# Performance work log

Hardware: AMD Instinct MI355X
Metric: run time of the kernel (lower is better)

## Reference

```python
import jax, jax.numpy as jnp
from jax import lax
import numpy as np

B, N, NPOINT, NSAMPLE, C = 4, 8192, 2048, 32, 128
RADIUS = 0.2
H1, H2, OUT = 64, 128, 128  # mlp: (3+C)->H1->H2, sas: H2->OUT


def fps(xyz, npoint):
    # furthest point sampling: xyz (B,N,3) -> idx (B,npoint) int32
    b, n, _ = xyz.shape
    init_idx = jnp.zeros((b,), jnp.int32)

    def step(carry, _):
        dist, last = carry
        p = jnp.take_along_axis(xyz, last[:, None, None], axis=1)  # (B,1,3)
        d = jnp.sum((xyz - p) ** 2, axis=-1)                       # (B,N)
        dist = jnp.minimum(dist, d)
        nxt = jnp.argmax(dist, axis=-1).astype(jnp.int32)
        return (dist, nxt), nxt

    (_, _), rest = lax.scan(step, (jnp.full((b, n), 1e10, jnp.float32), init_idx),
                            None, length=npoint - 1)
    return jnp.concatenate([init_idx[None, :], rest], axis=0).T    # (B,npoint)


def ball_query(xyz, new_xyz, radius, nsample):
    # xyz (B,N,3), new_xyz (B,S,3) -> idx (B,S,nsample) int32
    n = xyz.shape[1]
    d2 = jnp.sum((new_xyz[:, :, None, :] - xyz[:, None, :, :]) ** 2, axis=-1)  # (B,S,N)
    ar = jnp.arange(n, dtype=jnp.int32)
    keys = jnp.where(d2 <= radius * radius, ar, n)  # valid -> own index, invalid -> N
    neg_vals, _ = lax.top_k(-keys, nsample)          # smallest nsample keys
    idx = -neg_vals
    first = idx[..., :1]
    return jnp.where(idx >= n, first, idx)           # pad invalid with first valid


def gather_points(pts, idx):
    # pts (B,N,D), idx (B,S,ns) -> (B,S,ns,D)
    b, s, ns = idx.shape
    flat = jnp.take_along_axis(pts, idx.reshape(b, s * ns, 1), axis=1)
    return flat.reshape(b, s, ns, -1)


def setup_inputs() -> dict:
    key = jax.random.key(0)
    ks = jax.random.split(key, 8)
    xyz = jax.random.uniform(ks[0], (B, N, 3), dtype=jnp.float32)
    features = jax.random.normal(ks[1], (B, C, N), dtype=jnp.float32)
    cin = C + 3
    W1 = jax.random.normal(ks[2], (H1, cin), dtype=jnp.float32) / np.sqrt(cin)
    b1 = jnp.zeros((H1,), jnp.float32)
    W2 = jax.random.normal(ks[3], (H2, H1), dtype=jnp.float32) / np.sqrt(H1)
    b2 = jnp.zeros((H2,), jnp.float32)
    Wsa = jax.random.normal(ks[4], (OUT, H2), dtype=jnp.float32) / np.sqrt(H2)
    bsa = jnp.zeros((OUT,), jnp.float32)
    return {"xyz": xyz, "features": features, "W1": W1, "b1": b1,
            "W2": W2, "b2": b2, "Wsa": Wsa, "bsa": bsa}


def reference(xyz, features, W1, b1, W2, b2, Wsa, bsa):
    center_idx = fps(xyz, NPOINT)                                   # (B,S)
    new_xyz = jnp.take_along_axis(xyz, center_idx[:, :, None], axis=1)  # (B,S,3)
    g_idx = ball_query(xyz, new_xyz, RADIUS, NSAMPLE)               # (B,S,ns)
    g_xyz = gather_points(xyz, g_idx) - new_xyz[:, :, None, :]      # (B,S,ns,3) relative coords
    g_feat = gather_points(features.transpose(0, 2, 1), g_idx)      # (B,S,ns,C)
    h = jnp.concatenate([g_xyz, g_feat], axis=-1)                   # (B,S,ns,3+C)
    h = jax.nn.relu(jnp.einsum('bsnc,oc->bsno', h, W1) + b1)        # shared 1x1-conv MLP
    h = jax.nn.relu(jnp.einsum('bsnc,oc->bsno', h, W2) + b2)
    pooled = jnp.max(h, axis=2)                                     # max over nsample -> (B,S,H2)
    out = jnp.einsum('bsc,oc->bso', pooled, Wsa) + bsa              # sas channel mixer
    return new_xyz, out.transpose(0, 2, 1)                          # (B,S,3), (B,OUT,S)
```

## Files before the change

### kernel.cpp

```cpp
#include <hip/hip_runtime.h>
#include <cstdint>
#include <cstddef>

#define NB 4
#define NN 8192
#define NPTS 2048
#define NSAMP 32
#define NC 128
#define CIN 131
#define NH1 64
#define NH2 128
#define NOUTC 128
#define GCELLS 4096

typedef float v2f __attribute__((ext_vector_type(2)));

__device__ __forceinline__ float d2_exact(float ax, float ay, float az,
                                          float bx, float by, float bz) {
  float dx = ax - bx, dy = ay - by, dz = az - bz;
  return __fadd_rn(__fadd_rn(__fmul_rn(dx, dx), __fmul_rn(dy, dy)),
                   __fmul_rn(dz, dz));
}

#if __has_builtin(__builtin_amdgcn_mov_dpp)
template <int CTRL>
__device__ __forceinline__ float dppf(float v) {
  return __int_as_float(
      __builtin_amdgcn_mov_dpp(__float_as_int(v), CTRL, 0xF, 0xF, true));
}
template <int CTRL>
__device__ __forceinline__ int dppi(int v) {
  return __builtin_amdgcn_mov_dpp(v, CTRL, 0xF, 0xF, true);
}
#else
template <int CTRL>
__device__ __forceinline__ float dppf(float v) {
  const int m = (CTRL == 0xB1) ? 1 : (CTRL == 0x4E) ? 2 : (CTRL == 0x141) ? 7 : 15;
  return __shfl_xor(v, m);
}
template <int CTRL>
__device__ __forceinline__ int dppi(int v) {
  const int m = (CTRL == 0xB1) ? 1 : (CTRL == 0x4E) ? 2 : (CTRL == 0x141) ? 7 : 15;
  return __shfl_xor(v, m);
}
#endif

__device__ __forceinline__ bool tgt(float av, int ai, float bv, int bi) {
  return (av > bv) || (av == bv && ai < bi);
}

__device__ __forceinline__ void red_pair(float& bv, int& bi, float ov, int oi) {
  bool t = tgt(ov, oi, bv, bi);
  bv = t ? ov : bv;
  bi = t ? oi : bi;
}
template <int CTRL>
__device__ __forceinline__ void red5(float& v, int& i, float& x, float& y,
                                     float& z) {
  float ov = dppf<CTRL>(v);
  int oi = dppi<CTRL>(i);
  float ox = dppf<CTRL>(x), oy = dppf<CTRL>(y), oz = dppf<CTRL>(z);
  bool t = tgt(ov, oi, v, i);
  v = t ? ov : v; i = t ? oi : i;
  x = t ? ox : x; y = t ? oy : y; z = t ? oz : z;
}

__device__ __forceinline__ int spread3(int v) {
  return (v & 1) | ((v & 2) << 2) | ((v & 4) << 4) | ((v & 8) << 6);
}

__global__ __launch_bounds__(1024, 1) void sort_kernel(
    const float* __restrict__ xyz, float* __restrict__ xs,
    float* __restrict__ ys, float* __restrict__ zs, int* __restrict__ io) {
  __shared__ int hist[GCELLS];
  __shared__ int cbase[GCELLS];
  __shared__ int wtot[16];
  __shared__ int woff[16];
  const int b = blockIdx.x;
  const int tid = threadIdx.x;
  const int lane = tid & 63;
  const int wid = tid >> 6;
  const float* xb = xyz + (size_t)b * NN * 3;
  for (int i = tid; i < GCELLS; i += 1024) hist[i] = 0;
  __syncthreads();
  int cell[8];
  float px[8], py[8], pz[8];
#pragma unroll
  for (int k = 0; k < 8; ++k) {
    int j = tid + (k << 10);
    float x = xb[j * 3 + 0], y = xb[j * 3 + 1], z = xb[j * 3 + 2];
    px[k] = x; py[k] = y; pz[k] = z;
    int cx = min(15, max(0, (int)(x * 16.0f)));
    int cy = min(15, max(0, (int)(y * 16.0f)));
    int cz = min(15, max(0, (int)(z * 16.0f)));
    cell[k] = spread3(cx) | (spread3(cy) << 1) | (spread3(cz) << 2);
    atomicAdd(&hist[cell[k]], 1);
  }
  __syncthreads();
  const int i0 = tid * 4;
  int h0 = hist[i0], h1 = hist[i0 + 1], h2 = hist[i0 + 2], h3 = hist[i0 + 3];
  int s4 = h0 + h1 + h2 + h3;
  int v = s4;
#pragma unroll
  for (int d = 1; d < 64; d <<= 1) {
    int o = __shfl_up(v, d);
    if (lane >= d) v += o;
  }
  if (lane == 63) wtot[wid] = v;
  __syncthreads();
  if (tid < 16) {
    int acc = 0;
    for (int w = 0; w < 16; ++w) {
      if (w == tid) woff[tid] = acc;
      acc += wtot[w];
    }
  }
  __syncthreads();
  int eb = woff[wid] + v - s4;
  cbase[i0] = eb;
  cbase[i0 + 1] = eb + h0;
  cbase[i0 + 2] = eb + h0 + h1;
  cbase[i0 + 3] = eb + h0 + h1 + h2;
  __syncthreads();
  for (int i = tid; i < GCELLS; i += 1024) hist[i] = 0;
  __syncthreads();
  const size_t bo = (size_t)b * NN;
#pragma unroll
  for (int k = 0; k < 8; ++k) {
    int pos = cbase[cell[k]] + atomicAdd(&hist[cell[k]], 1);
    xs[bo + pos] = px[k];
    ys[bo + pos] = py[k];
    zs[bo + pos] = pz[k];
    io[bo + pos] = tid + (k << 10);
  }
}

__global__ __launch_bounds__(1024, 1) void fps_kernel(
    const float* __restrict__ xyz, const float* __restrict__ xs,
    const float* __restrict__ ys, const float* __restrict__ zs,
    const int* __restrict__ io, float* __restrict__ newxyz) {
#pragma clang fp contract(off)
  const int b = blockIdx.x;
  const int tid = threadIdx.x;
  const int lane = tid & 63;
  const int wid = tid >> 6;
  const size_t bo = (size_t)b * NN;

  float X[8], Y[8], Z[8], D[8];
  int I[8];
  float gcx, gcy, gcz, gr;
  {
    float mx = 0.f, my = 0.f, mz = 0.f;
#pragma unroll
    for (int k = 0; k < 8; ++k) {
      int s = tid * 8 + k;
      X[k] = xs[bo + s];
      Y[k] = ys[bo + s];
      Z[k] = zs[bo + s];
      I[k] = io[bo + s];
      D[k] = 1e30f;
      mx += X[k]; my += Y[k]; mz += Z[k];
    }
    mx *= 0.125f; my *= 0.125f; mz *= 0.125f;
    float r2m = 0.f;
#pragma unroll
    for (int k = 0; k < 8; ++k)
      r2m = fmaxf(r2m, d2_exact(X[k], Y[k], Z[k], mx, my, mz));
    gcx = mx; gcy = my; gcz = mz;
    gr = __fmul_rn(sqrtf(r2m), 1.0001f) + 1e-6f;
  }
  float gv = -1.0f;
  int gidx = 0x7fffffff;
  float gx = 0.f, gy = 0.f, gz = 0.f;
  float T = 3e38f;
  float cv = -1.0f; int ci = 0x7fffffff;
  float ccx = 0.f, ccy = 0.f, ccz = 0.f;

  __shared__ float sv[2][16];
  __shared__ int si[2][16];
  __shared__ float sxx[2][16], syy[2][16], szz[2][16];

  const float* xb = xyz + (size_t)b * NN * 3;
  float cx = xb[0], cy = xb[1], cz = xb[2];
  if (tid == 0) {
    newxyz[(size_t)b * NPTS * 3 + 0] = cx;
    newxyz[(size_t)b * NPTS * 3 + 1] = cy;
    newxyz[(size_t)b * NPTS * 3 + 2] = cz;
  }

  for (int t = 1; t < NPTS; ++t) {
    const int par = t & 1;
    const float d2c = d2_exact(gcx, gcy, gcz, cx, cy, cz);
    const bool dirty = d2c < T;
    if (__ballot(dirty) != 0ull) {
      float nv = -1.f; int ni = 0x7fffffff;
      float nx = 0.f, ny = 0.f, nz = 0.f;
#pragma unroll
      for (int k = 0; k < 8; ++k) {
        float dd = d2_exact(X[k], Y[k], Z[k], cx, cy, cz);
        float nd = fminf(D[k], dd);
        D[k] = nd;
        bool c = tgt(nd, I[k], nv, ni);
        nv = c ? nd : nv; ni = c ? I[k] : ni;
        nx = c ? X[k] : nx; ny = c ? Y[k] : ny; nz = c ? Z[k] : nz;
      }
      gv = nv; gidx = ni; gx = nx; gy = ny; gz = nz;
      float s = __fadd_rn(__fmul_rn(sqrtf(gv), 1.0001f),
                          __fadd_rn(gr, 2e-3f));
      T = __fmul_rn(__fmul_rn(s, s), 1.0001f);
      float rv = gv; int ri = gidx;
      red_pair(rv, ri, dppf<0xB1>(rv), dppi<0xB1>(ri));
      red_pair(rv, ri, dppf<0x4E>(rv), dppi<0x4E>(ri));
      red_pair(rv, ri, dppf<0x141>(rv), dppi<0x141>(ri));
      red_pair(rv, ri, dppf<0x140>(rv), dppi<0x140>(ri));
      red_pair(rv, ri, __shfl_xor(rv, 16), __shfl_xor(ri, 16));
      red_pair(rv, ri, __shfl_xor(rv, 32), __shfl_xor(ri, 32));
      unsigned long long m = __ballot(gidx == ri);
      int owner = (int)__builtin_ctzll(m);
      cv = rv; ci = ri;
      ccx = __shfl(gx, owner);
      ccy = __shfl(gy, owner);
      ccz = __shfl(gz, owner);
    }
    if (lane == 0) {
      sv[par][wid] = cv; si[par][wid] = ci;
      sxx[par][wid] = ccx; syy[par][wid] = ccy; szz[par][wid] = ccz;
    }
    __syncthreads();
    const int sl = lane & 15;
    float v = sv[par][sl];
    int i = si[par][sl];
    float xx = sxx[par][sl], yy = syy[par][sl], zz = szz[par][sl];
    red5<0xB1>(v, i, xx, yy, zz);
    red5<0x4E>(v, i, xx, yy, zz);
    red5<0x141>(v, i, xx, yy, zz);
    red5<0x140>(v, i, xx, yy, zz);
    cx = xx; cy = yy; cz = zz;
    if (gidx == i) {
      size_t o = ((size_t)b * NPTS + t) * 3;
      newxyz[o + 0] = xx; newxyz[o + 1] = yy; newxyz[o + 2] = zz;
    }
  }
}

__global__ __launch_bounds__(1024, 1) void fps_nosort_kernel(
    const float* __restrict__ xyz, float* __restrict__ newxyz) {
#pragma clang fp contract(off)
  const int b = blockIdx.x;
  const int tid = threadIdx.x;
  const int lane = tid & 63;
  const int wid = tid >> 6;
  const float* xb = xyz + (size_t)b * NN * 3;
  v2f x2[4], y2[4], z2[4], dd[4];
#pragma unroll
  for (int p = 0; p < 4; ++p) {
    int j0 = tid + ((2 * p) << 10);
    int j1 = tid + ((2 * p + 1) << 10);
    x2[p].x = xb[j0 * 3 + 0]; x2[p].y = xb[j1 * 3 + 0];
    y2[p].x = xb[j0 * 3 + 1]; y2[p].y = xb[j1 * 3 + 1];
    z2[p].x = xb[j0 * 3 + 2]; z2[p].y = xb[j1 * 3 + 2];
    dd[p].x = 1e10f; dd[p].y = 1e10f;
  }
  __shared__ float vbuf[2][16];
  __shared__ int ibuf[2][16];
  __shared__ float cbuf[2][16][3];
  float cx = xb[0], cy = xb[1], cz = xb[2];
  if (tid == 0) {
    newxyz[(size_t)b * NPTS * 3 + 0] = cx;
    newxyz[(size_t)b * NPTS * 3 + 1] = cy;
    newxyz[(size_t)b * NPTS * 3 + 2] = cz;
  }
  for (int t = 1; t < NPTS; ++t) {
    const int par = t & 1;
    float bv = -1.0f; int bi = 0;
    float bwx = 0.f, bwy = 0.f, bwz = 0.f;
#pragma unroll
    for (int p = 0; p < 4; ++p) {
      v2f dx = x2[p] - (v2f){cx, cx};
      v2f dy = y2[p] - (v2f){cy, cy};
      v2f dz = z2[p] - (v2f){cz, cz};
      v2f s = dx * dx + dy * dy + dz * dz;
      v2f nd;
      nd.x = fminf(dd[p].x, s.x);
      nd.y = fminf(dd[p].y, s.y);
      dd[p] = nd;
      { bool c = nd.x > bv;
        bv = c ? nd.x : bv; bi = c ? (tid + ((2 * p) << 10)) : bi;
        bwx = c ? x2[p].x : bwx; bwy = c ? y2[p].x : bwy; bwz = c ? z2[p].x : bwz; }
      { bool c = nd.y > bv;
        bv = c ? nd.y : bv; bi = c ? (tid + ((2 * p + 1) << 10)) : bi;
        bwx = c ? x2[p].y : bwx; bwy = c ? y2[p].y : bwy; bwz = c ? z2[p].y : bwz; }
    }
    red_pair(bv, bi, dppf<0xB1>(bv), dppi<0xB1>(bi));
    red_pair(bv, bi, dppf<0x4E>(bv), dppi<0x4E>(bi));
    red_pair(bv, bi, dppf<0x141>(bv), dppi<0x141>(bi));
    red_pair(bv, bi, dppf<0x140>(bv), dppi<0x140>(bi));
    red_pair(bv, bi, __shfl_xor(bv, 16), __shfl_xor(bi, 16));
    red_pair(bv, bi, __shfl_xor(bv, 32), __shfl_xor(bi, 32));
    if (tid == (bi & 1023)) {
      vbuf[par][wid] = bv; ibuf[par][wid] = bi;
      cbuf[par][wid][0] = bwx; cbuf[par][wid][1] = bwy; cbuf[par][wid][2] = bwz;
    }
    __syncthreads();
    float v2w = vbuf[par][lane & 15];
    int i2w = ibuf[par][lane & 15];
    red_pair(v2w, i2w, dppf<0xB1>(v2w), dppi<0xB1>(i2w));
    red_pair(v2w, i2w, dppf<0x4E>(v2w), dppi<0x4E>(i2w));
    red_pair(v2w, i2w, dppf<0x141>(v2w), dppi<0x141>(i2w));
    red_pair(v2w, i2w, dppf<0x140>(v2w), dppi<0x140>(i2w));
    const int slot = (i2w & 1023) >> 6;
    cx = cbuf[par][slot][0]; cy = cbuf[par][slot][1]; cz = cbuf[par][slot][2];
    if (tid == (i2w & 1023)) {
      size_t o = ((size_t)b * NPTS + t) * 3;
      newxyz[o + 0] = cx; newxyz[o + 1] = cy; newxyz[o + 2] = cz;
    }
  }
}

__global__ __launch_bounds__(256) void ballq_kernel(
    const float* __restrict__ xyz, const float* __restrict__ newxyz,
    int* __restrict__ bidx) {
  const int cid = blockIdx.x * 4 + (threadIdx.x >> 6);
  const int lane = threadIdx.x & 63;
  const int b = cid >> 11;
  const float* xb = xyz + (size_t)b * NN * 3;
  const float cx = newxyz[(size_t)cid * 3 + 0];
  const float cy = newxyz[(size_t)cid * 3 + 1];
  const float cz = newxyz[(size_t)cid * 3 + 2];
  int* ob = bidx + (size_t)cid * NSAMP;
  int total = 0;
  int first = -1;
  for (int c0 = 0; c0 < NN; c0 += 64) {
    int j = c0 + lane;
    float xx = xb[j * 3 + 0], yy = xb[j * 3 + 1], zz = xb[j * 3 + 2];
    float d2 = d2_exact(cx, cy, cz, xx, yy, zz);
    bool in = d2 <= 0.04f;
    unsigned long long m = __ballot(in);
    if (first < 0 && m) first = c0 + __builtin_ctzll(m);
    int pos = total + __popcll(m & ((1ull << lane) - 1ull));
    if (in && pos < NSAMP) ob[pos] = j;
    total += __popcll(m);
    if (total >= NSAMP) break;
  }
  if (total < NSAMP && lane < NSAMP - total) ob[total + lane] = first;
}

__global__ void tw_kernel(const float* __restrict__ W1, const float* __restrict__ W2,
                          const float* __restrict__ Wsa, float* __restrict__ w1t,
                          float* __restrict__ w2t, float* __restrict__ wsat) {
  int i = blockIdx.x * blockDim.x + threadIdx.x;
  if (i < CIN * NH1) w1t[i] = W1[(i % NH1) * CIN + (i / NH1)];
  if (i < NH1 * NH2) w2t[i] = W2[(i % NH2) * NH1 + (i / NH2)];
  if (i < NH2 * NOUTC) wsat[i] = Wsa[(i % NOUTC) * NH2 + (i / NOUTC)];
}

__global__ void tfeat_kernel(const float* __restrict__ feat, float* __restrict__ featT) {
  __shared__ float tile[32][33];
  const int b = blockIdx.z;
  const int n0 = blockIdx.x * 32, c0 = blockIdx.y * 32;
  const int tx = threadIdx.x, ty = threadIdx.y;
#pragma unroll
  for (int r = 0; r < 4; ++r)
    tile[ty + r * 8][tx] = feat[((size_t)b * NC + c0 + ty + r * 8) * NN + n0 + tx];
  __syncthreads();
#pragma unroll
  for (int r = 0; r < 4; ++r)
    featT[((size_t)b * NN + n0 + ty + r * 8) * NC + c0 + tx] = tile[tx][ty + r * 8];
}

#define HS 36
__global__ __launch_bounds__(256) void mlp_kernel(
    const float* __restrict__ xyz, const float* __restrict__ fsrc,
    const float* __restrict__ newxyz, const int* __restrict__ bidx,
    const float* __restrict__ w1t, const float* __restrict__ b1,
    const float* __restrict__ w2t, const float* __restrict__ b2,
    const float* __restrict__ wsat, const float* __restrict__ bsa,
    float* __restrict__ out1, int useT) {
  __shared__ float h[CIN * HS];
  __shared__ float h1[NH1 * HS];
  __shared__ float pl[256];
  __shared__ float pooled[NH2];
  __shared__ int sidx[NSAMP];
  __shared__ float sc[3];
  const int cid = blockIdx.x;
  const int b = cid >> 11;
  const int s = cid & 2047;
  const int tid = threadIdx.x;
  if (tid < NSAMP) sidx[tid] = bidx[(size_t)cid * NSAMP + tid];
  if (tid < 3) sc[tid] = newxyz[(size_t)cid * 3 + tid];
  __syncthreads();
  {
    const int ss = tid >> 3, q = tid & 7;
    const int j = sidx[ss];
    if (useT) {
      const float4* fr = (const float4*)(fsrc + ((size_t)b * NN + j) * NC + q * 16);
#pragma unroll
      for (int u = 0; u < 4; ++u) {
        float4 v = fr[u];
        int c = 3 + q * 16 + u * 4;
        h[(c + 0) * HS + ss] = v.x;
        h[(c + 1) * HS + ss] = v.y;
        h[(c + 2) * HS + ss] = v.z;
        h[(c + 3) * HS + ss] = v.w;
      }
    } else {
      for (int u = 0; u < 16; ++u) {
        int c = q * 16 + u;
        h[(3 + c) * HS + ss] = fsrc[((size_t)b * NC + c) * NN + j];
      }
    }
    if (q == 0) {
      const float* pr = xyz + ((size_t)b * NN + j) * 3;
      h[0 * HS + ss] = pr[0] - sc[0];
      h[1 * HS + ss] = pr[1] - sc[1];
      h[2 * HS + ss] = pr[2] - sc[2];
    }
  }
  __syncthreads();
  {
    const int o = tid & 63, sg = tid >> 6;
    float acc[8];
    const float bb = b1[o];
#pragma unroll
    for (int i = 0; i < 8; ++i) acc[i] = bb;
    const float4* hb = (const float4*)&h[sg * 8];
    for (int k = 0; k < CIN; ++k) {
      float w = w1t[k * NH1 + o];
      float4 a = hb[k * (HS / 4) + 0];
      float4 c = hb[k * (HS / 4) + 1];
      acc[0] = fmaf(w, a.x, acc[0]); acc[1] = fmaf(w, a.y, acc[1]);
      acc[2] = fmaf(w, a.z, acc[2]); acc[3] = fmaf(w, a.w, acc[3]);
      acc[4] = fmaf(w, c.x, acc[4]); acc[5] = fmaf(w, c.y, acc[5]);
      acc[6] = fmaf(w, c.z, acc[6]); acc[7] = fmaf(w, c.w, acc[7]);
    }
#pragma unroll
    for (int i = 0; i < 8; ++i) h1[o * HS + sg * 8 + i] = fmaxf(acc[i], 0.0f);
  }
  __syncthreads();
  {
    const int o = tid & 127, sg = tid >> 7;
    float acc[16];
    const float bb = b2[o];
#pragma unroll
    for (int i = 0; i < 16; ++i) acc[i] = bb;
    const float4* hb = (const float4*)&h1[sg * 16];
    for (int k = 0; k < NH1; ++k) {
      float w = w2t[k * NH2 + o];
#pragma unroll
      for (int u = 0; u < 4; ++u) {
        float4 a = hb[k * (HS / 4) + u];
        acc[u * 4 + 0] = fmaf(w, a.x, acc[u * 4 + 0]);
        acc[u * 4 + 1] = fmaf(w, a.y, acc[u * 4 + 1]);
        acc[u * 4 + 2] = fmaf(w, a.z, acc[u * 4 + 2]);
        acc[u * 4 + 3] = fmaf(w, a.w, acc[u * 4 + 3]);
      }
    }
    float pm = acc[0];
#pragma unroll
    for (int i = 1; i < 16; ++i) pm = fmaxf(pm, acc[i]);
    pl[sg * 128 + o] = pm;
  }
  __syncthreads();
  if (tid < NH2) pooled[tid] = fmaxf(fmaxf(pl[tid], pl[128 + tid]), 0.0f);
  __syncthreads();
  if (tid < NOUTC) {
    float acc = bsa[tid];
    for (int k = 0; k < NH2; ++k) acc = fmaf(pooled[k], wsat[k * NOUTC + tid], acc);
    out1[((size_t)b * NOUTC + tid) * NPTS + s] = acc;
  }
}

extern "C" void kernel_launch(void* const* d_in, const int* in_sizes, int n_in,
                              void* d_out, int out_size, void* d_ws, size_t ws_size,
                              hipStream_t stream) {
  const float* xyz = (const float*)d_in[0];
  const float* feat = (const float*)d_in[1];
  const float* W1 = (const float*)d_in[2];
  const float* b1 = (const float*)d_in[3];
  const float* W2 = (const float*)d_in[4];
  const float* b2 = (const float*)d_in[5];
  const float* Wsa = (const float*)d_in[6];
  const float* bsa = (const float*)d_in[7];
  float* out = (float*)d_out;
  float* newxyz = out;
  float* out1 = out + (size_t)NB * NPTS * 3;

  const size_t sort_f = (size_t)NB * NN * 4;
  const size_t small_f = (size_t)CIN * NH1 + NH1 * NH2 + NH2 * NOUTC +
                         (size_t)NB * NPTS * NSAMP;
  const size_t featT_f = (size_t)NB * NN * NC;

  float* ws = (float*)d_ws;
  bool useSort = ws_size >= (sort_f + small_f) * 4;
  bool useT = ws_size >= (sort_f + small_f + featT_f) * 4;

  float* xs = ws;
  float* ysr = xs + (size_t)NB * NN;
  float* zsr = ysr + (size_t)NB * NN;
  int* iosr = (int*)(zsr + (size_t)NB * NN);
  float* base2 = useSort ? (ws + sort_f) : ws;
  float* w1t = base2;
  float* w2t = w1t + CIN * NH1;
  float* wsat = w2t + NH1 * NH2;
  int* bidx = (int*)(wsat + NH2 * NOUTC);
  float* featT = (float*)(bidx + (size_t)NB * NPTS * NSAMP);

  tw_kernel<<<64, 256, 0, stream>>>(W1, W2, Wsa, w1t, w2t, wsat);
  if (useT)
    tfeat_kernel<<<dim3(NN / 32, NC / 32, NB), dim3(32, 8), 0, stream>>>(feat, featT);
  if (useSort) {
    sort_kernel<<<NB, 1024, 0, stream>>>(xyz, xs, ysr, zsr, iosr);
    fps_kernel<<<NB, 1024, 0, stream>>>(xyz, xs, ysr, zsr, iosr, newxyz);
  } else {
    fps_nosort_kernel<<<NB, 1024, 0, stream>>>(xyz, newxyz);
  }
  ballq_kernel<<<NB * NPTS / 4, 256, 0, stream>>>(xyz, newxyz, bidx);
  mlp_kernel<<<NB * NPTS, 256, 0, stream>>>(xyz, useT ? featT : feat, newxyz, bidx,
                                            w1t, b1, w2t, b2, wsat, bsa, out1,
                                            (int)useT);
}
```

Before: 3.709 ms.

## Simplify sorted FPS loop: drop dirty-skip, add wave-0 final reduce

New measurement: 3.838 ms. +3.5%, slower.

```diff
diff --git a/kernel.cpp b/kernel.cpp
--- a/kernel.cpp
+++ b/kernel.cpp
@@ -64,6 +64,17 @@
   v = t ? ov : v; i = t ? oi : i;
   x = t ? ox : x; y = t ? oy : y; z = t ? oz : z;
 }
+
+#define SEL8(A, kk, out)                      \
+  {                                           \
+    float s0_ = ((kk) & 1) ? A[1] : A[0];     \
+    float s1_ = ((kk) & 1) ? A[3] : A[2];     \
+    float s2_ = ((kk) & 1) ? A[5] : A[4];     \
+    float s3_ = ((kk) & 1) ? A[7] : A[6];     \
+    float s4_ = ((kk) & 2) ? s1_ : s0_;       \
+    float s5_ = ((kk) & 2) ? s3_ : s2_;       \
+    out = ((kk) & 4) ? s5_ : s4_;             \
+  }
 
 __device__ __forceinline__ int spread3(int v) {
   return (v & 1) | ((v & 2) << 2) | ((v & 4) << 4) | ((v & 8) << 6);
@@ -148,37 +159,20 @@
 
   float X[8], Y[8], Z[8], D[8];
   int I[8];
-  float gcx, gcy, gcz, gr;
-  {
-    float mx = 0.f, my = 0.f, mz = 0.f;
-#pragma unroll
-    for (int k = 0; k < 8; ++k) {
-      int s = tid * 8 + k;
-      X[k] = xs[bo + s];
-      Y[k] = ys[bo + s];
-      Z[k] = zs[bo + s];
-      I[k] = io[bo + s];
-      D[k] = 1e30f;
-      mx += X[k]; my += Y[k]; mz += Z[k];
-    }
-    mx *= 0.125f; my *= 0.125f; mz *= 0.125f;
-    float r2m = 0.f;
-#pragma unroll
-    for (int k = 0; k < 8; ++k)
-      r2m = fmaxf(r2m, d2_exact(X[k], Y[k], Z[k], mx, my, mz));
-    gcx = mx; gcy = my; gcz = mz;
-    gr = __fmul_rn(sqrtf(r2m), 1.0001f) + 1e-6f;
-  }
-  float gv = -1.0f;
-  int gidx = 0x7fffffff;
-  float gx = 0.f, gy = 0.f, gz = 0.f;
-  float T = 3e38f;
-  float cv = -1.0f; int ci = 0x7fffffff;
-  float ccx = 0.f, ccy = 0.f, ccz = 0.f;
-
-  __shared__ float sv[2][16];
-  __shared__ int si[2][16];
-  __shared__ float sxx[2][16], syy[2][16], szz[2][16];
+#pragma unroll
+  for (int k = 0; k < 8; ++k) {
+    int s = tid * 8 + k;
+    X[k] = xs[bo + s];
+    Y[k] = ys[bo + s];
+    Z[k] = zs[bo + s];
+    I[k] = io[bo + s];
+    D[k] = 1e30f;
+  }
+
+  __shared__ float sv[16];
+  __shared__ int si[16];
+  __shared__ float sx[16], sy[16], sz[16];
+  __shared__ float fin[3];
 
   const float* xb = xyz + (size_t)b * NN * 3;
   float cx = xb[0], cy = xb[1], cz = xb[2];
@@ -189,57 +183,62 @@
   }
 
   for (int t = 1; t < NPTS; ++t) {
-    const int par = t & 1;
-    const float d2c = d2_exact(gcx, gcy, gcz, cx, cy, cz);
-    const bool dirty = d2c < T;
-    if (__ballot(dirty) != 0ull) {
-      float nv = -1.f; int ni = 0x7fffffff;
-      float nx = 0.f, ny = 0.f, nz = 0.f;
-#pragma unroll
-      for (int k = 0; k < 8; ++k) {
-        float dd = d2_exact(X[k], Y[k], Z[k], cx, cy, cz);
-        float nd = fminf(D[k], dd);
-        D[k] = nd;
-        bool c = tgt(nd, I[k], nv, ni);
-        nv = c ? nd : nv; ni = c ? I[k] : ni;
-        nx = c ? X[k] : nx; ny = c ? Y[k] : ny; nz = c ? Z[k] : nz;
+    float bv = -1.0f;
+    int bi = 0x7fffffff;
+    int kw = 0;
+#pragma unroll
+    for (int k = 0; k < 8; ++k) {
+      float dd = d2_exact(X[k], Y[k], Z[k], cx, cy, cz);
+      float nd = fminf(D[k], dd);
+      D[k] = nd;
+      bool c = tgt(nd, I[k], bv, bi);
+      bv = c ? nd : bv;
+      bi = c ? I[k] : bi;
+      kw = c ? k : kw;
+    }
+    float rv = bv;
+    int ri = bi;
+    red_pair(rv, ri, dppf<0xB1>(rv), dppi<0xB1>(ri));
+    red_pair(rv, ri, dppf<0x4E>(rv), dppi<0x4E>(ri));
+    red_pair(rv, ri, dppf<0x141>(rv), dppi<0x141>(ri));
+    red_pair(rv, ri, dppf<0x140>(rv), dppi<0x140>(ri));
+    red_pair(rv, ri, __shfl_xor(rv, 16), __shfl_xor(ri, 16));
+    red_pair(rv, ri, __shfl_xor(rv, 32), __shfl_xor(ri, 32));
+    if (bi == ri) {
+      float ox, oy, oz;
+      SEL8(X, kw, ox);
+      SEL8(Y, kw, oy);
+      SEL8(Z, kw, oz);
+      sv[wid] = rv;
+      si[wid] = ri;
+      sx[wid] = ox;
+      sy[wid] = oy;
+      sz[wid] = oz;
+    }
+    __syncthreads();
+    if (wid == 0) {
+      const int e = lane & 15;
+      float v = sv[e];
+      int i = si[e];
+      float xx = sx[e], yy = sy[e], zz = sz[e];
+      red5<0xB1>(v, i, xx, yy, zz);
+      red5<0x4E>(v, i, xx, yy, zz);
+      red5<0x141>(v, i, xx, yy, zz);
+      red5<0x140>(v, i, xx, yy, zz);
+      if (lane == 0) {
+        fin[0] = xx;
+        fin[1] = yy;
+        fin[2] = zz;
+        size_t o = ((size_t)b * NPTS + t) * 3;
+        newxyz[o + 0] = xx;
+        newxyz[o + 1] = yy;
+        newxyz[o + 2] = zz;
       }
-      gv = nv; gidx = ni; gx = nx; gy = ny; gz = nz;
-      float s = __fadd_rn(__fmul_rn(sqrtf(gv), 1.0001f),
-                          __fadd_rn(gr, 2e-3f));
-      T = __fmul_rn(__fmul_rn(s, s), 1.0001f);
-      float rv = gv; int ri = gidx;
-      red_pair(rv, ri, dppf<0xB1>(rv), dppi<0xB1>(ri));
-      red_pair(rv, ri, dppf<0x4E>(rv), dppi<0x4E>(ri));
-      red_pair(rv, ri, dppf<0x141>(rv), dppi<0x141>(ri));
-      red_pair(rv, ri, dppf<0x140>(rv), dppi<0x140>(ri));
-      red_pair(rv, ri, __shfl_xor(rv, 16), __shfl_xor(ri, 16));
-      red_pair(rv, ri, __shfl_xor(rv, 32), __shfl_xor(ri, 32));
-      unsigned long long m = __ballot(gidx == ri);
-      int owner = (int)__builtin_ctzll(m);
-      cv = rv; ci = ri;
-      ccx = __shfl(gx, owner);
-      ccy = __shfl(gy, owner);
-      ccz = __shfl(gz, owner);
-    }
-    if (lane == 0) {
-      sv[par][wid] = cv; si[par][wid] = ci;
-      sxx[par][wid] = ccx; syy[par][wid] = ccy; szz[par][wid] = ccz;
     }
     __syncthreads();
-    const int sl = lane & 15;
-    float v = sv[par][sl];
-    int i = si[par][sl];
-    float xx = sxx[par][sl], yy = syy[par][sl], zz = szz[par][sl];
-    red5<0xB1>(v, i, xx, yy, zz);
-    red5<0x4E>(v, i, xx, yy, zz);
-    red5<0x141>(v, i, xx, yy, zz);
-    red5<0x140>(v, i, xx, yy, zz);
-    cx = xx; cy = yy; cz = zz;
-    if (gidx == i) {
-      size_t o = ((size_t)b * NPTS + t) * 3;
-      newxyz[o + 0] = xx; newxyz[o + 1] = yy; newxyz[o + 2] = zz;
-    }
+    cx = fin[0];
+    cy = fin[1];
+    cz = fin[2];
   }
 }
 
```
